# Kernel tuning notes

Hardware: AMD Instinct MI355X
Metric: run time of the kernel (lower is better)

The kernel has to match this reference:

```python
import jax, jax.numpy as jnp
import numpy as np
from jax import lax

B, S, V, E, H, NSEG = 64, 512, 50000, 512, 512, 64


def setup_inputs() -> dict:
    key = jax.random.key(0)
    ks = jax.random.split(key, 12)
    input_seqs = jax.random.randint(ks[0], (B, S), 1, V, dtype=jnp.int32)
    # pack_padded_sequence requires descending-sorted lengths; max len = S
    lens = np.sort(np.asarray(jax.random.randint(ks[1], (B,), S // 2, S + 1)))[::-1].copy()
    lens[0] = S
    input_lens = jnp.asarray(lens, dtype=jnp.int32)
    # layout[i]: NSEG+1 strictly increasing boundaries in [0, len_i]
    layout = jnp.asarray(np.stack([np.round(np.linspace(0.0, float(L), NSEG + 1)).astype(np.int32) for L in lens]))
    hidden = jnp.zeros((2, B, H), jnp.float32)  # unused by the original forward (rnn called without it)
    s = float(1.0 / np.sqrt(H))
    u = lambda k, shape: jax.random.uniform(k, shape, jnp.float32, -s, s)
    emb_table = (jax.random.normal(ks[2], (V, E), jnp.float32) * 0.02).at[0].set(0.0)  # padding_idx=0
    return {
        "input_seqs": input_seqs, "input_lens": input_lens, "hidden": hidden, "layout": layout,
        "emb_table": emb_table,
        "w_ih_f": u(ks[3], (3 * H, E)), "w_hh_f": u(ks[4], (3 * H, H)),
        "b_ih_f": u(ks[5], (3 * H,)), "b_hh_f": u(ks[6], (3 * H,)),
        "w_ih_b": u(ks[7], (3 * H, E)), "w_hh_b": u(ks[8], (3 * H, H)),
        "b_ih_b": u(ks[9], (3 * H,)), "b_hh_b": u(ks[10], (3 * H,)),
    }


def _gru_scan(xp, mask, w_hh, b_hh):
    """Single-direction GRU over precomputed input projections.
    xp: [B,S,3H] = x @ W_ih.T + b_ih, mask: [B,S] valid positions.
    Emulates packed sequence: state frozen and output zeroed past each length."""
    def step(h, inp):
        gx, m = inp                      # gx [B,3H], m [B,1]
        gh = h @ w_hh.T + b_hh           # [B,3H]
        xr, xz, xn = jnp.split(gx, 3, axis=-1)
        hr, hz, hn = jnp.split(gh, 3, axis=-1)
        r = jax.nn.sigmoid(xr + hr)
        z = jax.nn.sigmoid(xz + hz)
        n = jnp.tanh(xn + r * hn)
        h_new = (1.0 - z) * n + z * h
        h = jnp.where(m, h_new, h)
        return h, jnp.where(m, h_new, 0.0)
    h0 = jnp.zeros((xp.shape[0], w_hh.shape[1]), xp.dtype)
    hT, outs = lax.scan(step, h0, (xp.transpose(1, 0, 2), mask.T[:, :, None]))
    return hT, outs.transpose(1, 0, 2)   # [B,H], [B,S,H]


def _segment_max(context, layout, lens):
    """Ragged per-sample segment max: replaces the Python loops in getMaxedContext."""
    Bc, Sc, _ = context.shape
    t = jnp.arange(Sc)
    def per_sample(ctx, bnd, L):
        ids = jnp.searchsorted(bnd, t, side="right") - 1      # segment id of each position
        ids = jnp.where(t < L, ids, NSEG)                      # park padding in dump slot
        return jax.ops.segment_max(ctx, ids, num_segments=NSEG + 1)[:NSEG]
    return jax.vmap(per_sample)(context, layout, lens)         # [B,NSEG,D]


def _forward(input_seqs, input_lens, layout, emb_table,
             w_ih_f, w_hh_f, b_ih_f, b_hh_f, w_ih_b, w_hh_b, b_ih_b, b_hh_b):
    emb = emb_table.at[0].set(0.0)                  # padding_idx=0: row 0 fixed at zero, no grad
    x = emb[input_seqs]                             # [B,S,E]
    t = jnp.arange(S)
    mask = t[None, :] < input_lens[:, None]         # [B,S]
    # forward direction
    xp_f = x @ w_ih_f.T + b_ih_f                    # [B,S,3H]
    h_f, out_f = _gru_scan(xp_f, mask, w_hh_f, b_hh_f)
    # backward direction: reverse each sequence within its own length
    rev_idx = jnp.where(mask, input_lens[:, None] - 1 - t[None, :], t[None, :])
    x_rev = jnp.take_along_axis(x, rev_idx[:, :, None], axis=1)
    xp_b = x_rev @ w_ih_b.T + b_ih_b
    h_b, out_b_rev = _gru_scan(xp_b, mask, w_hh_b, b_hh_b)
    out_b = jnp.where(mask[:, :, None], jnp.take_along_axis(out_b_rev, rev_idx[:, :, None], axis=1), 0.0)
    context = jnp.concatenate([out_f, out_b], axis=-1)   # [B,S,2H]
    context = lax.stop_gradient(context)                  # original does context.detach()
    pooled = _segment_max(context, layout, input_lens)    # [B,NSEG,2H]
    h_stack = jnp.stack([h_f, h_b], axis=0)               # [num_dir,B,H]
    return pooled, h_stack


def reference(input_seqs, input_lens, hidden, layout, emb_table,
              w_ih_f, w_hh_f, b_ih_f, b_hh_f, w_ih_b, w_hh_b, b_ih_b, b_hh_b):
    # `hidden` is unused, matching the original (self.rnn(packed) ignores it)
    return _forward(input_seqs, input_lens, layout, emb_table,
                    w_ih_f, w_hh_f, b_ih_f, b_hh_f, w_ih_b, w_hh_b, b_ih_b, b_hh_b)
```

## Files before the change

### kernel.cpp

```cpp
#include <hip/hip_runtime.h>

typedef unsigned short u16;
typedef __attribute__((ext_vector_type(8))) short short8;
typedef __attribute__((ext_vector_type(4))) short short4v;
typedef __attribute__((ext_vector_type(4))) float f32x4;

#define B_    64
#define S_    512
#define E_    512
#define H_    512
#define NSEG_ 64

__device__ __forceinline__ float bf2f(u16 u) {
    union { unsigned int i; float f; } x; x.i = ((unsigned int)u) << 16; return x.f;
}
__device__ __forceinline__ u16 f2bf(float f) {
    union { float f; unsigned int i; } x; x.f = f;
    unsigned int r = x.i + 0x7fffu + ((x.i >> 16) & 1u);
    return (u16)(r >> 16);
}
__device__ __forceinline__ f32x4 mfma16(short8 a, short8 b, f32x4 c) {
    return __builtin_amdgcn_mfma_f32_16x16x32_bf16(a, b, c, 0, 0, 0);
}
__device__ __forceinline__ float sigmoidf_(float x) { return 1.f / (1.f + __expf(-x)); }
__device__ __forceinline__ float tanhf_(float x) {
    float e = __expf(-2.f * fabsf(x));
    float t = (1.f - e) / (1.f + e);
    return x < 0.f ? -t : t;
}

#define EMBB_OFF  0
#define WIHB_OFF  51200000
#define WHHB_OFF  54345728
#define HBUF_OFF  57491456
#define CNT_OFF   57753600
#define XP_OFF    57757696

__global__ __launch_bounds__(256) void prep_kernel(
    const float* __restrict__ emb,
    const float* __restrict__ wih_f, const float* __restrict__ whh_f,
    const float* __restrict__ wih_b, const float* __restrict__ whh_b,
    u16* __restrict__ embb, u16* __restrict__ wihbb, u16* __restrict__ whhbb,
    u16* __restrict__ hbuf, int* __restrict__ cnt)
{
    const int nt = gridDim.x * 256;
    const int i = blockIdx.x * 256 + threadIdx.x;

    const float4* e4 = (const float4*)emb;
    short4v* eo = (short4v*)embb;
    for (int k = i; k < 6400000; k += nt) {
        float4 v = e4[k];
        short4v o = { (short)f2bf(v.x), (short)f2bf(v.y), (short)f2bf(v.z), (short)f2bf(v.w) };
        eo[k] = o;
    }
    const float4* wf[4] = { (const float4*)wih_f, (const float4*)wih_b,
                            (const float4*)whh_f, (const float4*)whh_b };
    short4v* wo[4] = { (short4v*)wihbb, (short4v*)(wihbb + 786432),
                       (short4v*)whhbb, (short4v*)(whhbb + 786432) };
#pragma unroll
    for (int a = 0; a < 4; ++a) {
        for (int k = i; k < 196608; k += nt) {
            float4 v = wf[a][k];
            short4v o = { (short)f2bf(v.x), (short)f2bf(v.y), (short)f2bf(v.z), (short)f2bf(v.w) };
            wo[a][k] = o;
        }
    }
    int* hz = (int*)hbuf;
    for (int k = i; k < 65536; k += nt) hz[k] = 0;
    for (int k = i; k < 1024; k += nt) cnt[k] = 0;
}

__global__ __launch_bounds__(256) void proj_kernel(
    const int* __restrict__ seq, const u16* __restrict__ embb,
    const u16* __restrict__ wihbb,
    const float* __restrict__ b_ih_f, const float* __restrict__ b_ih_b,
    u16* __restrict__ xp)
{
    const int bid = blockIdx.x;
    const int mt = bid / 24, nt = bid % 24;
    const int tid = threadIdx.x;
    const int w = tid >> 6, l = tid & 63;
    const int q = l >> 4, col = l & 15;
    const int M0 = mt * 128 + (w >> 1) * 64;
    const int N0 = nt * 128 + (w & 1) * 64;

    const u16* arow[4];
#pragma unroll
    for (int ai = 0; ai < 4; ++ai) {
        const int tok = seq[M0 + ai * 16 + col];
        arow[ai] = embb + (long)tok * E_;
    }
    const u16* brow[4];
#pragma unroll
    for (int bi = 0; bi < 4; ++bi)
        brow[bi] = wihbb + (long)(N0 + bi * 16 + col) * E_;

    f32x4 acc[4][4];
#pragma unroll
    for (int ai = 0; ai < 4; ++ai)
#pragma unroll
        for (int bi = 0; bi < 4; ++bi) acc[ai][bi] = (f32x4){0,0,0,0};

    for (int k = 0; k < 16; ++k) {
        const int ko = k * 32 + q * 8;
        short8 a[4], b[4];
#pragma unroll
        for (int ai = 0; ai < 4; ++ai) a[ai] = *(const short8*)(arow[ai] + ko);
#pragma unroll
        for (int bi = 0; bi < 4; ++bi) b[bi] = *(const short8*)(brow[bi] + ko);
#pragma unroll
        for (int ai = 0; ai < 4; ++ai)
#pragma unroll
            for (int bi = 0; bi < 4; ++bi)
                acc[ai][bi] = mfma16(a[ai], b[bi], acc[ai][bi]);
    }

#pragma unroll
    for (int bi = 0; bi < 4; ++bi) {
        const int n = N0 + bi * 16 + col;
        const int dir = (n >= 1536) ? 1 : 0;
        const int j = n - dir * 1536;
        const int g = j >> 9, u = j & 511, uc = u >> 4;
        const float bias = dir ? b_ih_b[j] : b_ih_f[j];
        const long base = (long)(dir * 32 + uc) * (64L * 512 * 48) + g * 16 + col;
#pragma unroll
        for (int ai = 0; ai < 4; ++ai) {
#pragma unroll
            for (int i = 0; i < 4; ++i) {
                const int m = M0 + ai * 16 + q * 4 + i;
                const int bs = m >> 9, s = m & 511;
                xp[base + ((long)bs * 512 + s) * 48] = f2bf(acc[ai][bi][i] + bias);
            }
        }
    }
}

__global__ __launch_bounds__(64, 1) void rnn_kernel(
    const int* __restrict__ lens, const int* __restrict__ layout,
    const u16* __restrict__ whhbb,
    const float* __restrict__ b_hh_f, const float* __restrict__ b_hh_b,
    const u16* __restrict__ xp, u16* __restrict__ hbuf, int* __restrict__ cnt,
    float* __restrict__ out)
{
    const int bid = blockIdx.x;
    const int dir = bid >> 7;
    const int g   = (bid >> 5) & 3;
    const int uc  = bid & 31;
    const int u0  = uc * 16;
    const int l = threadIdx.x;
    const int q = l >> 4, col = l & 15;
    const int u = u0 + col;

    const u16* Whh = whhbb + (long)dir * (3 * H_ * H_);
    short8 wreg[16][3];
#pragma unroll
    for (int k = 0; k < 16; ++k)
#pragma unroll
        for (int gg = 0; gg < 3; ++gg)
            wreg[k][gg] = *(const short8*)(Whh + (long)(gg * 512 + u0 + col) * H_ + k * 32 + q * 8);

    const float* bhh = dir ? b_hh_b : b_hh_f;
    const float bh0 = bhh[0 * 512 + u];
    const float bh1 = bhh[1 * 512 + u];
    const float bh2 = bhh[2 * 512 + u];

    int samp[4], Ls[4], seg[4], bnd[4];
    float hm[4], mx[4];
    bool done[4];
#pragma unroll
    for (int i = 0; i < 4; ++i) {
        samp[i] = g * 16 + q * 4 + i;
        Ls[i] = lens[samp[i]];
        hm[i] = 0.f;
        mx[i] = -3.4e38f;
        done[i] = false;
        if (dir == 0) { seg[i] = 0; bnd[i] = layout[samp[i] * 65 + 1]; }
        else          { seg[i] = 63; bnd[i] = layout[samp[i] * 65 + 63]; }
    }
    const int asamp = g * 16 + col;

    const u16* xpb = xp + (long)(dir * 32 + uc) * (64L * 512 * 48);
    u16* hb_base = hbuf + (long)dir * 2 * B_ * H_;
    int* fl = cnt + (dir * 4 + g) * 32;

    u16 cxr[4], cxz[4], cxn[4];
    int cpv[4]; bool cval[4];
#pragma unroll
    for (int i = 0; i < 4; ++i) {
        const int L = Ls[i];
        cval[i] = (0 < L);
        int p = dir ? (L - 1) : 0;
        if (p < 0) p = 0;
        cpv[i] = p;
        const u16* xq = xpb + ((long)samp[i] * 512 + p) * 48;
        cxr[i] = xq[0 * 16 + col];
        cxz[i] = xq[1 * 16 + col];
        cxn[i] = xq[2 * 16 + col];
    }

    for (int t = 0; t < 512; ++t) {
        if (t > 0) {
            unsigned long long rdy;
            do {
                const int v = __hip_atomic_load(&fl[l & 31], __ATOMIC_RELAXED,
                                                __HIP_MEMORY_SCOPE_SYSTEM);
                rdy = __ballot((l >= 32) || (v >= t));
                if (rdy != ~0ULL) __builtin_amdgcn_s_sleep(1);
            } while (rdy != ~0ULL);
            (void)__hip_atomic_load(&fl[0], __ATOMIC_ACQUIRE, __HIP_MEMORY_SCOPE_SYSTEM);
        }

        const u16* hr = hb_base + (long)(t & 1) * B_ * H_ + (long)asamp * H_;
        short8 afrag[16];
#pragma unroll
        for (int k = 0; k < 16; ++k)
            afrag[k] = *(const short8*)(hr + k * 32 + q * 8);

        u16 nxr[4], nxz[4], nxn[4];
        int npv[4]; bool nval[4];
        const int tn = t + 1;
        if (tn < 512) {
#pragma unroll
            for (int i = 0; i < 4; ++i) {
                const int L = Ls[i];
                nval[i] = (tn < L);
                int p = dir ? (L - 1 - tn) : tn;
                if (p < 0) p = 0;
                npv[i] = p;
                const u16* xq = xpb + ((long)samp[i] * 512 + p) * 48;
                nxr[i] = xq[0 * 16 + col];
                nxz[i] = xq[1 * 16 + col];
                nxn[i] = xq[2 * 16 + col];
            }
        } else {
#pragma unroll
            for (int i = 0; i < 4; ++i) { nxr[i] = nxz[i] = nxn[i] = 0; npv[i] = 0; nval[i] = false; }
        }

        f32x4 ar = {0,0,0,0}, az = {0,0,0,0}, an = {0,0,0,0};
#pragma unroll
        for (int k = 0; k < 16; ++k) {
            ar = mfma16(afrag[k], wreg[k][0], ar);
            az = mfma16(afrag[k], wreg[k][1], az);
            an = mfma16(afrag[k], wreg[k][2], an);
        }

        float hnv[4];
#pragma unroll
        for (int i = 0; i < 4; ++i) {
            const float r = sigmoidf_(bf2f(cxr[i]) + ar[i] + bh0);
            const float z = sigmoidf_(bf2f(cxz[i]) + az[i] + bh1);
            const float n = tanhf_(bf2f(cxn[i]) + r * (an[i] + bh2));
            const float hnew = (1.f - z) * n + z * hm[i];
            if (cval[i]) hm[i] = hnew;
            hnv[i] = hnew;
        }

        u16* hw = hb_base + (long)((t + 1) & 1) * B_ * H_;
#pragma unroll
        for (int i = 0; i < 4; ++i) {
            const float other = __shfl_xor(hm[i], 1);
            if ((col & 1) == 0) {
                const unsigned int pk = ((unsigned int)f2bf(other) << 16) | (unsigned int)f2bf(hm[i]);
                __hip_atomic_store((unsigned int*)(hw + (long)samp[i] * H_ + u), pk,
                                   __ATOMIC_RELAXED, __HIP_MEMORY_SCOPE_SYSTEM);
            }
        }

        asm volatile("s_waitcnt vmcnt(0)" ::: "memory");
        if (l == 0)
            __hip_atomic_store(&fl[uc], t + 1, __ATOMIC_RELAXED, __HIP_MEMORY_SCOPE_SYSTEM);

#pragma unroll
        for (int i = 0; i < 4; ++i) {
            if (cval[i]) {
                if (dir == 0) {
                    while (t >= bnd[i] && seg[i] < 63) {
                        out[((long)samp[i] * 64 + seg[i]) * 1024 + u] = mx[i];
                        seg[i]++;
                        bnd[i] = layout[samp[i] * 65 + seg[i] + 1];
                        mx[i] = -3.4e38f;
                    }
                } else {
                    while (cpv[i] < bnd[i] && seg[i] > 0) {
                        out[((long)samp[i] * 64 + seg[i]) * 1024 + 512 + u] = mx[i];
                        seg[i]--;
                        bnd[i] = layout[samp[i] * 65 + seg[i]];
                        mx[i] = -3.4e38f;
                    }
                }
                mx[i] = fmaxf(mx[i], hnv[i]);
            } else if (!done[i]) {
                out[((long)samp[i] * 64 + seg[i]) * 1024 + dir * 512 + u] = mx[i];
                done[i] = true;
            }
        }

#pragma unroll
        for (int i = 0; i < 4; ++i) {
            cxr[i] = nxr[i]; cxz[i] = nxz[i]; cxn[i] = nxn[i];
            cpv[i] = npv[i]; cval[i] = nval[i];
        }
    }

#pragma unroll
    for (int i = 0; i < 4; ++i) {
        if (!done[i])
            out[((long)samp[i] * 64 + seg[i]) * 1024 + dir * 512 + u] = mx[i];
        out[4194304 + dir * (B_ * H_) + samp[i] * H_ + u] = hm[i];
    }
}

extern "C" void kernel_launch(void* const* d_in, const int* in_sizes, int n_in,
                              void* d_out, int out_size, void* d_ws, size_t ws_size,
                              hipStream_t stream) {
    const int*   seq    = (const int*)d_in[0];
    const int*   lens   = (const int*)d_in[1];
    const int*   layout = (const int*)d_in[3];
    const float* emb    = (const float*)d_in[4];
    const float* w_ih_f = (const float*)d_in[5];
    const float* w_hh_f = (const float*)d_in[6];
    const float* b_ih_f = (const float*)d_in[7];
    const float* b_hh_f = (const float*)d_in[8];
    const float* w_ih_b = (const float*)d_in[9];
    const float* w_hh_b = (const float*)d_in[10];
    const float* b_ih_b = (const float*)d_in[11];
    const float* b_hh_b = (const float*)d_in[12];
    float* out = (float*)d_out;
    char* ws = (char*)d_ws;

    u16* embb  = (u16*)(ws + EMBB_OFF);
    u16* wihbb = (u16*)(ws + WIHB_OFF);
    u16* whhbb = (u16*)(ws + WHHB_OFF);
    u16* hbuf  = (u16*)(ws + HBUF_OFF);
    int* cnt   = (int*)(ws + CNT_OFF);
    u16* xp    = (u16*)(ws + XP_OFF);

    prep_kernel<<<2048, 256, 0, stream>>>(emb, w_ih_f, w_hh_f, w_ih_b, w_hh_b,
                                          embb, wihbb, whhbb, hbuf, cnt);
    proj_kernel<<<256 * 24, 256, 0, stream>>>(seq, embb, wihbb, b_ih_f, b_ih_b, xp);
    rnn_kernel<<<256, 64, 0, stream>>>(lens, layout, whhbb, b_hh_f, b_hh_b,
                                       xp, hbuf, cnt, out);
}
```

Measured before the change: 2.582 ms.

## Interleave two independent batch-group chains per block in GRU recurrence

Each recurrent block now handles two batch groups, alternating a phase for each every timestep, so the launch drops from 256 to 128 blocks and the weights held in registers are shared by both chains. While one chain waits on its flag barrier, the other's work can hide the latency. The h-state loads become inline-asm global loads with sc0 sc1 cache bypass, the explicit acquire load is removed, and the next-step x projection fetch moves after the pooling. The per-block serial work doubles and register pressure rises, and dropping the acquire load relies on the cache-bypassing loads for memory ordering.

After: 4.157 ms. 61.0% more time.

```diff
diff --git a/kernel.cpp b/kernel.cpp
--- a/kernel.cpp
+++ b/kernel.cpp
@@ -135,6 +135,143 @@
     }
 }
 
+
+#define DECL_CHAIN(PX, GRP) \
+    int PX##samp[4], PX##Ls[4], PX##seg[4], PX##bnd[4]; \
+    float PX##hm[4], PX##mx[4]; \
+    bool PX##done[4]; \
+    u16 PX##cxr[4], PX##cxz[4], PX##cxn[4]; \
+    int PX##cpv[4]; bool PX##cval[4]; \
+    const int PX##g = (GRP); \
+    const int PX##asamp = PX##g * 16 + col; \
+    int* PX##fl = cnt + (dir * 4 + PX##g) * 32; \
+    _Pragma("unroll") \
+    for (int i = 0; i < 4; ++i) { \
+        PX##samp[i] = PX##g * 16 + q * 4 + i; \
+        PX##Ls[i] = lens[PX##samp[i]]; \
+        PX##hm[i] = 0.f; PX##mx[i] = -3.4e38f; PX##done[i] = false; \
+        if (dir == 0) { PX##seg[i] = 0;  PX##bnd[i] = layout[PX##samp[i] * 65 + 1]; } \
+        else          { PX##seg[i] = 63; PX##bnd[i] = layout[PX##samp[i] * 65 + 63]; } \
+        const int L = PX##Ls[i]; \
+        PX##cval[i] = (0 < L); \
+        int p = dir ? (L - 1) : 0; if (p < 0) p = 0; \
+        PX##cpv[i] = p; \
+        const u16* xq = xpb + ((long)PX##samp[i] * 512 + p) * 48; \
+        PX##cxr[i] = xq[0 * 16 + col]; \
+        PX##cxz[i] = xq[1 * 16 + col]; \
+        PX##cxn[i] = xq[2 * 16 + col]; \
+    }
+
+#define RNN_PHASE(PX, t) do { \
+    if ((t) > 0) { \
+        unsigned long long rdy; \
+        do { \
+            const int v = __hip_atomic_load(&PX##fl[l & 31], __ATOMIC_RELAXED, \
+                                            __HIP_MEMORY_SCOPE_SYSTEM); \
+            rdy = __ballot((l >= 32) || (v >= (t))); \
+            if (rdy != ~0ULL) __builtin_amdgcn_s_sleep(1); \
+        } while (rdy != ~0ULL); \
+    } \
+    const u16* hr = hb_base + (long)((t) & 1) * B_ * H_ + (long)PX##asamp * H_ + q * 8; \
+    short8 afrag[16]; \
+    asm volatile("global_load_dwordx4 %0, %1, off sc0 sc1"             : "=&v"(afrag[0])  : "v"(hr)); \
+    asm volatile("global_load_dwordx4 %0, %1, off offset:64 sc0 sc1"   : "=&v"(afrag[1])  : "v"(hr)); \
+    asm volatile("global_load_dwordx4 %0, %1, off offset:128 sc0 sc1"  : "=&v"(afrag[2])  : "v"(hr)); \
+    asm volatile("global_load_dwordx4 %0, %1, off offset:192 sc0 sc1"  : "=&v"(afrag[3])  : "v"(hr)); \
+    asm volatile("global_load_dwordx4 %0, %1, off offset:256 sc0 sc1"  : "=&v"(afrag[4])  : "v"(hr)); \
+    asm volatile("global_load_dwordx4 %0, %1, off offset:320 sc0 sc1"  : "=&v"(afrag[5])  : "v"(hr)); \
+    asm volatile("global_load_dwordx4 %0, %1, off offset:384 sc0 sc1"  : "=&v"(afrag[6])  : "v"(hr)); \
+    asm volatile("global_load_dwordx4 %0, %1, off offset:448 sc0 sc1"  : "=&v"(afrag[7])  : "v"(hr)); \
+    asm volatile("global_load_dwordx4 %0, %1, off offset:512 sc0 sc1"  : "=&v"(afrag[8])  : "v"(hr)); \
+    asm volatile("global_load_dwordx4 %0, %1, off offset:576 sc0 sc1"  : "=&v"(afrag[9])  : "v"(hr)); \
+    asm volatile("global_load_dwordx4 %0, %1, off offset:640 sc0 sc1"  : "=&v"(afrag[10]) : "v"(hr)); \
+    asm volatile("global_load_dwordx4 %0, %1, off offset:704 sc0 sc1"  : "=&v"(afrag[11]) : "v"(hr)); \
+    asm volatile("global_load_dwordx4 %0, %1, off offset:768 sc0 sc1"  : "=&v"(afrag[12]) : "v"(hr)); \
+    asm volatile("global_load_dwordx4 %0, %1, off offset:832 sc0 sc1"  : "=&v"(afrag[13]) : "v"(hr)); \
+    asm volatile("global_load_dwordx4 %0, %1, off offset:896 sc0 sc1"  : "=&v"(afrag[14]) : "v"(hr)); \
+    asm volatile("global_load_dwordx4 %0, %1, off offset:960 sc0 sc1"  : "=&v"(afrag[15]) : "v"(hr)); \
+    asm volatile("s_waitcnt vmcnt(0)" ::: "memory"); \
+    __builtin_amdgcn_sched_barrier(0); \
+    f32x4 ar = {0,0,0,0}, az = {0,0,0,0}, an = {0,0,0,0}; \
+    _Pragma("unroll") \
+    for (int k = 0; k < 16; ++k) { \
+        ar = mfma16(afrag[k], wreg[0][k], ar); \
+        az = mfma16(afrag[k], wreg[1][k], az); \
+        an = mfma16(afrag[k], wreg[2][k], an); \
+    } \
+    float hnv[4]; \
+    _Pragma("unroll") \
+    for (int i = 0; i < 4; ++i) { \
+        const float r = sigmoidf_(bf2f(PX##cxr[i]) + ar[i] + bh0); \
+        const float z = sigmoidf_(bf2f(PX##cxz[i]) + az[i] + bh1); \
+        const float n = tanhf_(bf2f(PX##cxn[i]) + r * (an[i] + bh2)); \
+        const float hnew = (1.f - z) * n + z * PX##hm[i]; \
+        if (PX##cval[i]) PX##hm[i] = hnew; \
+        hnv[i] = hnew; \
+    } \
+    u16* hw = hb_base + (long)(((t) + 1) & 1) * B_ * H_; \
+    _Pragma("unroll") \
+    for (int i = 0; i < 4; ++i) { \
+        const float other = __shfl_xor(PX##hm[i], 1); \
+        if ((col & 1) == 0) { \
+            const unsigned int pk = ((unsigned int)f2bf(other) << 16) | (unsigned int)f2bf(PX##hm[i]); \
+            __hip_atomic_store((unsigned int*)(hw + (long)PX##samp[i] * H_ + u), pk, \
+                               __ATOMIC_RELAXED, __HIP_MEMORY_SCOPE_SYSTEM); \
+        } \
+    } \
+    asm volatile("s_waitcnt vmcnt(0)" ::: "memory"); \
+    if (l == 0) \
+        __hip_atomic_store(&PX##fl[uc], (t) + 1, __ATOMIC_RELAXED, __HIP_MEMORY_SCOPE_SYSTEM); \
+    _Pragma("unroll") \
+    for (int i = 0; i < 4; ++i) { \
+        if (PX##cval[i]) { \
+            if (dir == 0) { \
+                while ((t) >= PX##bnd[i] && PX##seg[i] < 63) { \
+                    out[((long)PX##samp[i] * 64 + PX##seg[i]) * 1024 + u] = PX##mx[i]; \
+                    PX##seg[i]++; \
+                    PX##bnd[i] = layout[PX##samp[i] * 65 + PX##seg[i] + 1]; \
+                    PX##mx[i] = -3.4e38f; \
+                } \
+            } else { \
+                while (PX##cpv[i] < PX##bnd[i] && PX##seg[i] > 0) { \
+                    out[((long)PX##samp[i] * 64 + PX##seg[i]) * 1024 + 512 + u] = PX##mx[i]; \
+                    PX##seg[i]--; \
+                    PX##bnd[i] = layout[PX##samp[i] * 65 + PX##seg[i]]; \
+                    PX##mx[i] = -3.4e38f; \
+                } \
+            } \
+            PX##mx[i] = fmaxf(PX##mx[i], hnv[i]); \
+        } else if (!PX##done[i]) { \
+            out[((long)PX##samp[i] * 64 + PX##seg[i]) * 1024 + dir * 512 + u] = PX##mx[i]; \
+            PX##done[i] = true; \
+        } \
+    } \
+    const int tn = (t) + 1; \
+    if (tn < 512) { \
+        _Pragma("unroll") \
+        for (int i = 0; i < 4; ++i) { \
+            const int L = PX##Ls[i]; \
+            PX##cval[i] = (tn < L); \
+            int p = dir ? (L - 1 - tn) : tn; \
+            if (p < 0) p = 0; \
+            PX##cpv[i] = p; \
+            const u16* xq = xpb + ((long)PX##samp[i] * 512 + p) * 48; \
+            PX##cxr[i] = xq[0 * 16 + col]; \
+            PX##cxz[i] = xq[1 * 16 + col]; \
+            PX##cxn[i] = xq[2 * 16 + col]; \
+        } \
+    } \
+} while (0)
+
+#define RNN_FLUSH(PX) do { \
+    _Pragma("unroll") \
+    for (int i = 0; i < 4; ++i) { \
+        if (!PX##done[i]) \
+            out[((long)PX##samp[i] * 64 + PX##seg[i]) * 1024 + dir * 512 + u] = PX##mx[i]; \
+        out[4194304 + dir * (B_ * H_) + PX##samp[i] * H_ + u] = PX##hm[i]; \
+    } \
+} while (0)
+
 __global__ __launch_bounds__(64, 1) void rnn_kernel(
     const int* __restrict__ lens, const int* __restrict__ layout,
     const u16* __restrict__ whhbb,
@@ -143,8 +280,8 @@
     float* __restrict__ out)
 {
     const int bid = blockIdx.x;
-    const int dir = bid >> 7;
-    const int g   = (bid >> 5) & 3;
+    const int dir = bid >> 6;
+    const int pr  = (bid >> 5) & 1;
     const int uc  = bid & 31;
     const int u0  = uc * 16;
     const int l = threadIdx.x;
@@ -152,163 +289,38 @@
     const int u = u0 + col;
 
     const u16* Whh = whhbb + (long)dir * (3 * H_ * H_);
-    short8 wreg[16][3];
-#pragma unroll
-    for (int k = 0; k < 16; ++k)
-#pragma unroll
-        for (int gg = 0; gg < 3; ++gg)
-            wreg[k][gg] = *(const short8*)(Whh + (long)(gg * 512 + u0 + col) * H_ + k * 32 + q * 8);
+    short8 wreg[3][16];
+#pragma unroll
+    for (int gg = 0; gg < 3; ++gg) {
+        const u16* wr = Whh + (long)(gg * 512 + u0 + col) * H_ + q * 8;
+#pragma unroll
+        for (int k = 0; k < 16; ++k)
+            wreg[gg][k] = *(const short8*)(wr + k * 32);
+    }
+#pragma unroll
+    for (int gg = 0; gg < 3; ++gg)
+#pragma unroll
+        for (int k = 0; k < 16; ++k)
+            asm volatile("" : "+v"(wreg[gg][k]));
 
     const float* bhh = dir ? b_hh_b : b_hh_f;
     const float bh0 = bhh[0 * 512 + u];
     const float bh1 = bhh[1 * 512 + u];
     const float bh2 = bhh[2 * 512 + u];
 
-    int samp[4], Ls[4], seg[4], bnd[4];
-    float hm[4], mx[4];
-    bool done[4];
-#pragma unroll
-    for (int i = 0; i < 4; ++i) {
-        samp[i] = g * 16 + q * 4 + i;
-        Ls[i] = lens[samp[i]];
-        hm[i] = 0.f;
-        mx[i] = -3.4e38f;
-        done[i] = false;
-        if (dir == 0) { seg[i] = 0; bnd[i] = layout[samp[i] * 65 + 1]; }
-        else          { seg[i] = 63; bnd[i] = layout[samp[i] * 65 + 63]; }
-    }
-    const int asamp = g * 16 + col;
-
     const u16* xpb = xp + (long)(dir * 32 + uc) * (64L * 512 * 48);
     u16* hb_base = hbuf + (long)dir * 2 * B_ * H_;
-    int* fl = cnt + (dir * 4 + g) * 32;
-
-    u16 cxr[4], cxz[4], cxn[4];
-    int cpv[4]; bool cval[4];
-#pragma unroll
-    for (int i = 0; i < 4; ++i) {
-        const int L = Ls[i];
-        cval[i] = (0 < L);
-        int p = dir ? (L - 1) : 0;
-        if (p < 0) p = 0;
-        cpv[i] = p;
-        const u16* xq = xpb + ((long)samp[i] * 512 + p) * 48;
-        cxr[i] = xq[0 * 16 + col];
-        cxz[i] = xq[1 * 16 + col];
-        cxn[i] = xq[2 * 16 + col];
-    }
+
+    DECL_CHAIN(A_, pr * 2)
+    DECL_CHAIN(B_, pr * 2 + 1)
 
     for (int t = 0; t < 512; ++t) {
-        if (t > 0) {
-            unsigned long long rdy;
-            do {
-                const int v = __hip_atomic_load(&fl[l & 31], __ATOMIC_RELAXED,
-                                                __HIP_MEMORY_SCOPE_SYSTEM);
-                rdy = __ballot((l >= 32) || (v >= t));
-                if (rdy != ~0ULL) __builtin_amdgcn_s_sleep(1);
-            } while (rdy != ~0ULL);
-            (void)__hip_atomic_load(&fl[0], __ATOMIC_ACQUIRE, __HIP_MEMORY_SCOPE_SYSTEM);
-        }
-
-        const u16* hr = hb_base + (long)(t & 1) * B_ * H_ + (long)asamp * H_;
-        short8 afrag[16];
-#pragma unroll
-        for (int k = 0; k < 16; ++k)
-            afrag[k] = *(const short8*)(hr + k * 32 + q * 8);
-
-        u16 nxr[4], nxz[4], nxn[4];
-        int npv[4]; bool nval[4];
-        const int tn = t + 1;
-        if (tn < 512) {
-#pragma unroll
-            for (int i = 0; i < 4; ++i) {
-                const int L = Ls[i];
-                nval[i] = (tn < L);
-                int p = dir ? (L - 1 - tn) : tn;
-                if (p < 0) p = 0;
-                npv[i] = p;
-                const u16* xq = xpb + ((long)samp[i] * 512 + p) * 48;
-                nxr[i] = xq[0 * 16 + col];
-                nxz[i] = xq[1 * 16 + col];
-                nxn[i] = xq[2 * 16 + col];
-            }
-        } else {
-#pragma unroll
-            for (int i = 0; i < 4; ++i) { nxr[i] = nxz[i] = nxn[i] = 0; npv[i] = 0; nval[i] = false; }
-        }
-
-        f32x4 ar = {0,0,0,0}, az = {0,0,0,0}, an = {0,0,0,0};
-#pragma unroll
-        for (int k = 0; k < 16; ++k) {
-            ar = mfma16(afrag[k], wreg[k][0], ar);
-            az = mfma16(afrag[k], wreg[k][1], az);
-            an = mfma16(afrag[k], wreg[k][2], an);
-        }
-
-        float hnv[4];
-#pragma unroll
-        for (int i = 0; i < 4; ++i) {
-            const float r = sigmoidf_(bf2f(cxr[i]) + ar[i] + bh0);
-            const float z = sigmoidf_(bf2f(cxz[i]) + az[i] + bh1);
-            const float n = tanhf_(bf2f(cxn[i]) + r * (an[i] + bh2));
-            const float hnew = (1.f - z) * n + z * hm[i];
-            if (cval[i]) hm[i] = hnew;
-            hnv[i] = hnew;
-        }
-
-        u16* hw = hb_base + (long)((t + 1) & 1) * B_ * H_;
-#pragma unroll
-        for (int i = 0; i < 4; ++i) {
-            const float other = __shfl_xor(hm[i], 1);
-            if ((col & 1) == 0) {
-                const unsigned int pk = ((unsigned int)f2bf(other) << 16) | (unsigned int)f2bf(hm[i]);
-                __hip_atomic_store((unsigned int*)(hw + (long)samp[i] * H_ + u), pk,
-                                   __ATOMIC_RELAXED, __HIP_MEMORY_SCOPE_SYSTEM);
-            }
-        }
-
-        asm volatile("s_waitcnt vmcnt(0)" ::: "memory");
-        if (l == 0)
-            __hip_atomic_store(&fl[uc], t + 1, __ATOMIC_RELAXED, __HIP_MEMORY_SCOPE_SYSTEM);
-
-#pragma unroll
-        for (int i = 0; i < 4; ++i) {
-            if (cval[i]) {
-                if (dir == 0) {
-                    while (t >= bnd[i] && seg[i] < 63) {
-                        out[((long)samp[i] * 64 + seg[i]) * 1024 + u] = mx[i];
-                        seg[i]++;
-                        bnd[i] = layout[samp[i] * 65 + seg[i] + 1];
-                        mx[i] = -3.4e38f;
-                    }
-                } else {
-                    while (cpv[i] < bnd[i] && seg[i] > 0) {
-                        out[((long)samp[i] * 64 + seg[i]) * 1024 + 512 + u] = mx[i];
-                        seg[i]--;
-                        bnd[i] = layout[samp[i] * 65 + seg[i]];
-                        mx[i] = -3.4e38f;
-                    }
-                }
-                mx[i] = fmaxf(mx[i], hnv[i]);
-            } else if (!done[i]) {
-                out[((long)samp[i] * 64 + seg[i]) * 1024 + dir * 512 + u] = mx[i];
-                done[i] = true;
-            }
-        }
-
-#pragma unroll
-        for (int i = 0; i < 4; ++i) {
-            cxr[i] = nxr[i]; cxz[i] = nxz[i]; cxn[i] = nxn[i];
-            cpv[i] = npv[i]; cval[i] = nval[i];
-        }
-    }
-
-#pragma unroll
-    for (int i = 0; i < 4; ++i) {
-        if (!done[i])
-            out[((long)samp[i] * 64 + seg[i]) * 1024 + dir * 512 + u] = mx[i];
-        out[4194304 + dir * (B_ * H_) + samp[i] * H_ + u] = hm[i];
-    }
+        RNN_PHASE(A_, t);
+        RNN_PHASE(B_, t);
+    }
+
+    RNN_FLUSH(A_);
+    RNN_FLUSH(B_);
 }
 
 extern "C" void kernel_launch(void* const* d_in, const int* in_sizes, int n_in,
@@ -339,6 +351,6 @@
     prep_kernel<<<2048, 256, 0, stream>>>(emb, w_ih_f, w_hh_f, w_ih_b, w_hh_b,
                                           embb, wihbb, whhbb, hbuf, cnt);
     proj_kernel<<<256 * 24, 256, 0, stream>>>(seq, embb, wihbb, b_ih_f, b_ih_b, xp);
-    rnn_kernel<<<256, 64, 0, stream>>>(lens, layout, whhbb, b_hh_f, b_hh_b,
+    rnn_kernel<<<128, 64, 0, stream>>>(lens, layout, whhbb, b_hh_f, b_hh_b,
                                        xp, hbuf, cnt, out);
 }
```
